# Performance work log

Hardware: AMD Instinct MI355X
Metric: run time of the kernel (lower is better)

The kernel has to match this reference:

```python
import jax, jax.numpy as jnp
import numpy as np

D_MODEL = 1024
H = 16
D_K = D_MODEL // H
B = 2
S = 2048
NEG = -1000000000.0


def setup_inputs() -> dict:
    key = jax.random.key(0)
    ks = jax.random.split(key, 11)
    sc = 1.0 / np.sqrt(D_MODEL)
    inp = {
        "q": jax.random.normal(ks[0], (B, S, D_MODEL), jnp.float32),
        "k": jax.random.normal(ks[1], (B, S, D_MODEL), jnp.float32),
        "v": jax.random.normal(ks[2], (B, S, D_MODEL), jnp.float32),
        "mask": jnp.tril(jnp.ones((S, S), jnp.int32))[None, None, :, :],  # causal [1,1,S,S]
        "Wq": jax.random.normal(ks[3], (D_MODEL, D_MODEL), jnp.float32) * sc,
        "bq": jnp.zeros((D_MODEL,), jnp.float32),
        "Wk": jax.random.normal(ks[4], (D_MODEL, D_MODEL), jnp.float32) * sc,
        "bk": jnp.zeros((D_MODEL,), jnp.float32),
        "Wv": jax.random.normal(ks[5], (D_MODEL, D_MODEL), jnp.float32) * sc,
        "bv": jnp.zeros((D_MODEL,), jnp.float32),
        "Wo": jax.random.normal(ks[6], (D_MODEL, D_MODEL), jnp.float32) * sc,
        "bo": jnp.zeros((D_MODEL,), jnp.float32),
    }
    return inp


def reference(q, k, v, mask, Wq, bq, Wk, bk, Wv, bv, Wo, bo):
    # Linear projections (torch Linear: x @ W.T + b)
    query = q @ Wq.T + bq
    key_ = k @ Wk.T + bk
    value = v @ Wv.T + bv
    # [B,S,D] -> [B,H,S,Dk]
    def split_heads(x):
        return x.reshape(B, S, H, D_K).transpose(0, 2, 1, 3)
    query, key_, value = split_heads(query), split_heads(key_), split_heads(value)
    # scaled dot-product attention, scores [B,H,S,S]
    scores = jnp.einsum("bhqd,bhkd->bhqk", query, key_) / jnp.sqrt(
        jnp.asarray(D_K, query.dtype))
    scores = jnp.where(mask == 0, jnp.asarray(NEG, scores.dtype), scores)
    attn = jax.nn.softmax(scores, axis=-1)
    x = jnp.einsum("bhqk,bhkd->bhqd", attn, value)
    # merge heads [B,H,S,Dk] -> [B,S,D]
    x = x.transpose(0, 2, 1, 3).reshape(B, S, D_MODEL)
    return x @ Wo.T + bo
```

## Files before the change

### kernel.cpp

```cpp
#include <hip/hip_runtime.h>
#include <stdint.h>

#define D_MODEL 1024
#define NHEAD   16
#define DKH     64
#define NB      2
#define SSEQ    2048

typedef unsigned short u16;
typedef __bf16 bf16x8 __attribute__((ext_vector_type(8)));
typedef float  f32x4  __attribute__((ext_vector_type(4)));
typedef u16    u16x8  __attribute__((ext_vector_type(8)));

__device__ __forceinline__ u16 f2bf(float x) {
  union { float f; uint32_t u; } c; c.f = x;
  uint32_t r = c.u + 0x7FFFu + ((c.u >> 16) & 1u);
  return (u16)(r >> 16);
}

__device__ __forceinline__ void gload_lds16(const void* gsrc, void* ldsdst) {
  typedef const __attribute__((address_space(1))) uint32_t* gp_t;
  typedef __attribute__((address_space(3))) uint32_t* lp_t;
  gp_t g = reinterpret_cast<gp_t>(reinterpret_cast<uintptr_t>(gsrc));
  lp_t l = reinterpret_cast<lp_t>(reinterpret_cast<uintptr_t>(ldsdst));
  __builtin_amdgcn_global_load_lds(g, l, 16, 0, 0);
}

__device__ __forceinline__ f32x4 mfma16(bf16x8 a, bf16x8 b, f32x4 c) {
  return __builtin_amdgcn_mfma_f32_16x16x32_bf16(a, b, c, 0, 0, 0);
}

__device__ __forceinline__ bf16x8 lds_frag(const u16* tile, int row, int kelem) {
  int chunk = (kelem >> 3) ^ (row & 7);
  return *reinterpret_cast<const bf16x8*>(
      reinterpret_cast<const char*>(tile) + row * 128 + chunk * 16);
}

template<int NROWS>
__device__ __forceinline__ void stage_tile(const u16* __restrict__ g, int row0, int ldk,
                                           int k0, u16* ldsbase, int wid, int lane) {
  constexpr int CPW = NROWS / 32;
  #pragma unroll
  for (int i = 0; i < CPW; ++i) {
    int c = wid * CPW + i;
    int row = c * 8 + (lane >> 3);
    int cchunk = (lane & 7) ^ (lane >> 3);
    const u16* src = g + (size_t)(row0 + row) * ldk + k0 + cchunk * 8;
    gload_lds16(src, reinterpret_cast<char*>(ldsbase) + c * 1024);
  }
}

__global__ __launch_bounds__(256) void cast_kernel(
    const float* __restrict__ s0, const float* __restrict__ s1,
    const float* __restrict__ s2, const float* __restrict__ s3,
    u16* __restrict__ d0, u16* __restrict__ d1, u16* __restrict__ d2, u16* __restrict__ d3,
    int n8) {
  const int z = blockIdx.z;
  const float* s = (z == 0) ? s0 : (z == 1) ? s1 : (z == 2) ? s2 : s3;
  u16* d = (z == 0) ? d0 : (z == 1) ? d1 : (z == 2) ? d2 : d3;
  int i = blockIdx.x * 256 + threadIdx.x;
  if (i >= n8) return;
  float4 a = reinterpret_cast<const float4*>(s)[2 * i];
  float4 b = reinterpret_cast<const float4*>(s)[2 * i + 1];
  u16x8 o;
  o[0] = f2bf(a.x); o[1] = f2bf(a.y); o[2] = f2bf(a.z); o[3] = f2bf(a.w);
  o[4] = f2bf(b.x); o[5] = f2bf(b.y); o[6] = f2bf(b.z); o[7] = f2bf(b.w);
  reinterpret_cast<u16x8*>(d)[i] = o;
}

__device__ __forceinline__ void gemm_core(const u16* __restrict__ A, const u16* __restrict__ W,
                                          u16* ldsA, u16* ldsB, int brow, int bcol,
                                          f32x4 acc[4][4]) {
  const int tid = threadIdx.x;
  const int lane = tid & 63;
  const int wid = tid >> 6;
  const int wr = wid >> 1;
  const int wc = wid & 1;
  f32x4 z4 = {0.f, 0.f, 0.f, 0.f};
  #pragma unroll
  for (int i = 0; i < 4; ++i)
    #pragma unroll
    for (int j = 0; j < 4; ++j) acc[i][j] = z4;

  stage_tile<128>(A, brow, D_MODEL, 0, ldsA, wid, lane);
  stage_tile<128>(W, bcol, D_MODEL, 0, ldsB, wid, lane);
  __syncthreads();
  int buf = 0;
  const int KT = D_MODEL / 64;
  for (int kt = 0; kt < KT; ++kt) {
    if (kt + 1 < KT) {
      stage_tile<128>(A, brow, D_MODEL, (kt + 1) * 64, ldsA + (buf ^ 1) * 8192, wid, lane);
      stage_tile<128>(W, bcol, D_MODEL, (kt + 1) * 64, ldsB + (buf ^ 1) * 8192, wid, lane);
    }
    const u16* tA = ldsA + buf * 8192;
    const u16* tB = ldsB + buf * 8192;
    #pragma unroll
    for (int kk = 0; kk < 2; ++kk) {
      const int ke = kk * 32 + ((lane >> 4) << 3);
      bf16x8 af[4], bf[4];
      #pragma unroll
      for (int i = 0; i < 4; ++i) af[i] = lds_frag(tA, wr * 64 + i * 16 + (lane & 15), ke);
      #pragma unroll
      for (int j = 0; j < 4; ++j) bf[j] = lds_frag(tB, wc * 64 + j * 16 + (lane & 15), ke);
      __builtin_amdgcn_s_setprio(1);
      #pragma unroll
      for (int i = 0; i < 4; ++i)
        #pragma unroll
        for (int j = 0; j < 4; ++j) acc[i][j] = mfma16(af[i], bf[j], acc[i][j]);
      __builtin_amdgcn_s_setprio(0);
    }
    __syncthreads();
    buf ^= 1;
  }
}

__global__ __launch_bounds__(256) void gemm_qkv(
    const u16* __restrict__ x0, const u16* __restrict__ x1, const u16* __restrict__ x2,
    const u16* __restrict__ w0, const u16* __restrict__ w1, const u16* __restrict__ w2,
    const float* __restrict__ b0, const float* __restrict__ b1, const float* __restrict__ b2,
    u16* __restrict__ o0, u16* __restrict__ o1, u16* __restrict__ o2) {
  __shared__ u16 ldsA[2 * 128 * 64];
  __shared__ u16 ldsB[2 * 128 * 64];
  const int z = blockIdx.z;
  const u16* X = (z == 0) ? x0 : (z == 1) ? x1 : x2;
  const u16* W = (z == 0) ? w0 : (z == 1) ? w1 : w2;
  const float* bias = (z == 0) ? b0 : (z == 1) ? b1 : b2;
  u16* O = (z == 0) ? o0 : (z == 1) ? o1 : o2;
  const float scale = (z == 0) ? 0.125f : 1.0f;
  const int brow = blockIdx.y * 128;
  const int bcol = blockIdx.x * 128;
  f32x4 acc[4][4];
  gemm_core(X, W, ldsA, ldsB, brow, bcol, acc);
  const int lane = threadIdx.x & 63;
  const int wid = threadIdx.x >> 6;
  const int wr = wid >> 1, wc = wid & 1;
  #pragma unroll
  for (int j = 0; j < 4; ++j) {
    const int n = bcol + wc * 64 + j * 16 + (lane & 15);
    const float bn = bias[n];
    const int h = n >> 6, d = n & 63;
    #pragma unroll
    for (int i = 0; i < 4; ++i)
      #pragma unroll
      for (int r = 0; r < 4; ++r) {
        const int m = brow + wr * 64 + i * 16 + ((lane >> 4) << 2) + r;
        const int bb = m >> 11, s = m & (SSEQ - 1);
        O[(((size_t)(bb * NHEAD + h) * SSEQ + s) << 6) + d] = f2bf((acc[i][j][r] + bn) * scale);
      }
  }
}

__global__ __launch_bounds__(256) void gemm_out(const u16* __restrict__ A,
                                                const u16* __restrict__ W,
                                                const float* __restrict__ bias,
                                                float* __restrict__ out) {
  __shared__ u16 ldsA[2 * 128 * 64];
  __shared__ u16 ldsB[2 * 128 * 64];
  const int brow = blockIdx.y * 128;
  const int bcol = blockIdx.x * 128;
  f32x4 acc[4][4];
  gemm_core(A, W, ldsA, ldsB, brow, bcol, acc);
  const int lane = threadIdx.x & 63;
  const int wid = threadIdx.x >> 6;
  const int wr = wid >> 1, wc = wid & 1;
  #pragma unroll
  for (int j = 0; j < 4; ++j) {
    const int n = bcol + wc * 64 + j * 16 + (lane & 15);
    const float bn = bias[n];
    #pragma unroll
    for (int i = 0; i < 4; ++i)
      #pragma unroll
      for (int r = 0; r < 4; ++r) {
        const int m = brow + wr * 64 + i * 16 + ((lane >> 4) << 2) + r;
        out[(size_t)m * D_MODEL + n] = acc[i][j][r] + bn;
      }
  }
}

__global__ __launch_bounds__(256) void transpose_v(const u16* __restrict__ V,
                                                   u16* __restrict__ Vt) {
  __shared__ u16 t[64][72];
  const int tid = threadIdx.x;
  const int bh = blockIdx.y;
  const int s0 = blockIdx.x * 64;
  const u16* Vb = V + ((size_t)bh * SSEQ + s0) * DKH;
  const int row = tid >> 2;
  const int cg = (tid & 3) * 16;
  uint4 a = *reinterpret_cast<const uint4*>(Vb + (size_t)row * DKH + cg);
  uint4 b = *reinterpret_cast<const uint4*>(Vb + (size_t)row * DKH + cg + 8);
  *reinterpret_cast<uint4*>(&t[row][cg]) = a;
  *reinterpret_cast<uint4*>(&t[row][cg + 8]) = b;
  __syncthreads();
  const int d = tid >> 2;
  const int sg = (tid & 3) * 16;
  u16 vals[16];
  #pragma unroll
  for (int j = 0; j < 16; ++j) vals[j] = t[sg + j][d];
  u16* dst = Vt + ((size_t)bh * DKH + d) * SSEQ + s0 + sg;
  *reinterpret_cast<uint4*>(dst) = *reinterpret_cast<uint4*>(&vals[0]);
  *reinterpret_cast<uint4*>(dst + 8) = *reinterpret_cast<uint4*>(&vals[8]);
}

__device__ __forceinline__ void attn_strip(const u16* __restrict__ Qb,
                                           const u16* __restrict__ Kb,
                                           const u16* __restrict__ Vb,
                                           u16* __restrict__ ctxb,
                                           u16* myP, int strip, int lane) {
  const int g = lane >> 4;
  const int q0 = strip * 16;
  const int nt = (strip >> 2) + 1;
  const u16* Qp = Qb + (size_t)(q0 + (lane & 15)) * DKH + (g << 3);
  bf16x8 qf0 = *reinterpret_cast<const bf16x8*>(Qp);
  bf16x8 qf1 = *reinterpret_cast<const bf16x8*>(Qp + 32);

  f32x4 z4 = {0.f, 0.f, 0.f, 0.f};
  f32x4 acc[4] = {z4, z4, z4, z4};
  float mrow[4] = {-1e30f, -1e30f, -1e30f, -1e30f};
  float lrow[4] = {0.f, 0.f, 0.f, 0.f};

  bf16x8 kf[8], vf[8];
  #pragma unroll
  for (int jk = 0; jk < 4; ++jk)
    #pragma unroll
    for (int c = 0; c < 2; ++c)
      kf[jk * 2 + c] = *reinterpret_cast<const bf16x8*>(
          Kb + (size_t)(jk * 16 + (lane & 15)) * DKH + c * 32 + (g << 3));

  for (int t = 0; t < nt; ++t) {
    #pragma unroll
    for (int j = 0; j < 4; ++j)
      #pragma unroll
      for (int c = 0; c < 2; ++c)
        vf[j * 2 + c] = *reinterpret_cast<const bf16x8*>(
            Vb + (size_t)(j * 16 + (lane & 15)) * SSEQ + t * 64 + c * 32 + (g << 3));
    f32x4 sf[4];
    __builtin_amdgcn_s_setprio(1);
    #pragma unroll
    for (int jk = 0; jk < 4; ++jk) {
      f32x4 s = mfma16(qf0, kf[jk * 2 + 0], z4);
      sf[jk] = mfma16(qf1, kf[jk * 2 + 1], s);
    }
    __builtin_amdgcn_s_setprio(0);
    if (t + 1 < nt) {
      #pragma unroll
      for (int jk = 0; jk < 4; ++jk)
        #pragma unroll
        for (int c = 0; c < 2; ++c)
          kf[jk * 2 + c] = *reinterpret_cast<const bf16x8*>(
              Kb + (size_t)((t + 1) * 64 + jk * 16 + (lane & 15)) * DKH + c * 32 + (g << 3));
    }
    if (t == nt - 1) {
      #pragma unroll
      for (int jk = 0; jk < 4; ++jk)
        #pragma unroll
        for (int r = 0; r < 4; ++r) {
          int kv = t * 64 + jk * 16 + (lane & 15);
          int qrow = q0 + g * 4 + r;
          if (kv > qrow) sf[jk][r] = -1e9f;
        }
    }
    float scl[4];
    #pragma unroll
    for (int r = 0; r < 4; ++r) {
      float mx = fmaxf(fmaxf(sf[0][r], sf[1][r]), fmaxf(sf[2][r], sf[3][r]));
      #pragma unroll
      for (int dd = 1; dd < 16; dd <<= 1) mx = fmaxf(mx, __shfl_xor(mx, dd));
      float mn = fmaxf(mrow[r], mx);
      scl[r] = __expf(mrow[r] - mn);
      mrow[r] = mn;
      lrow[r] *= scl[r];
    }
    float rsum[4] = {0.f, 0.f, 0.f, 0.f};
    #pragma unroll
    for (int jk = 0; jk < 4; ++jk)
      #pragma unroll
      for (int r = 0; r < 4; ++r) {
        float p = __expf(sf[jk][r] - mrow[r]);
        rsum[r] += p;
        int row = g * 4 + r;
        int col = jk * 16 + (lane & 15);
        int chunk = (col >> 3) ^ (row & 7);
        *reinterpret_cast<u16*>(reinterpret_cast<char*>(myP) + row * 128 + chunk * 16 +
                                (col & 7) * 2) = f2bf(p);
      }
    #pragma unroll
    for (int r = 0; r < 4; ++r) {
      float s = rsum[r];
      #pragma unroll
      for (int dd = 1; dd < 16; dd <<= 1) s += __shfl_xor(s, dd);
      lrow[r] += s;
    }
    #pragma unroll
    for (int j = 0; j < 4; ++j)
      #pragma unroll
      for (int r = 0; r < 4; ++r) acc[j][r] *= scl[r];
    #pragma unroll
    for (int c = 0; c < 2; ++c) {
      bf16x8 pf = lds_frag(myP, lane & 15, c * 32 + (g << 3));
      __builtin_amdgcn_s_setprio(1);
      #pragma unroll
      for (int j = 0; j < 4; ++j) acc[j] = mfma16(pf, vf[j * 2 + c], acc[j]);
      __builtin_amdgcn_s_setprio(0);
    }
  }
  float inv[4];
  #pragma unroll
  for (int r = 0; r < 4; ++r) inv[r] = 1.0f / lrow[r];
  #pragma unroll
  for (int j = 0; j < 4; ++j)
    #pragma unroll
    for (int r = 0; r < 4; ++r) {
      int qrow = q0 + g * 4 + r;
      int d = j * 16 + (lane & 15);
      ctxb[(size_t)qrow * D_MODEL + d] = f2bf(acc[j][r] * inv[r]);
    }
}

__global__ __launch_bounds__(256) void attn_kernel(const u16* __restrict__ Q,
                                                   const u16* __restrict__ K,
                                                   const u16* __restrict__ Vt,
                                                   u16* __restrict__ ctx) {
  __shared__ u16 ldsP[4 * 16 * 64];
  const int lane = threadIdx.x & 63;
  const int wid = threadIdx.x >> 6;
  const int L = blockIdx.x + 16 * blockIdx.y;
  const int bh = ((L & 7) << 2) | ((L >> 3) & 3);
  const int p = (((L >> 5) & 15) << 2) | wid;
  const u16* Qb = Q + (size_t)bh * SSEQ * DKH;
  const u16* Kb = K + (size_t)bh * SSEQ * DKH;
  const u16* Vb = Vt + (size_t)bh * DKH * SSEQ;
  u16* ctxb = ctx + (size_t)(bh >> 4) * SSEQ * D_MODEL + (bh & 15) * DKH;
  u16* myP = ldsP + wid * 1024;
  attn_strip(Qb, Kb, Vb, ctxb, myP, 127 - p, lane);
  attn_strip(Qb, Kb, Vb, ctxb, myP, p, lane);
}

extern "C" void kernel_launch(void* const* d_in, const int* in_sizes, int n_in,
                              void* d_out, int out_size, void* d_ws, size_t ws_size,
                              hipStream_t stream) {
  const float* q  = (const float*)d_in[0];
  const float* k  = (const float*)d_in[1];
  const float* v  = (const float*)d_in[2];
  const float* Wq = (const float*)d_in[4];
  const float* bq = (const float*)d_in[5];
  const float* Wk = (const float*)d_in[6];
  const float* bk = (const float*)d_in[7];
  const float* Wv = (const float*)d_in[8];
  const float* bv = (const float*)d_in[9];
  const float* Wo = (const float*)d_in[10];
  const float* bo = (const float*)d_in[11];

  char* ws = (char*)d_ws;
  const size_t SZ_QKV = (size_t)NB * SSEQ * D_MODEL * 2;
  const size_t SZ_W   = (size_t)D_MODEL * D_MODEL * 2;
  u16* qb  = (u16*)(ws);
  u16* kb  = (u16*)(ws + SZ_QKV);
  u16* vb  = (u16*)(ws + 2 * SZ_QKV);
  u16* wqb = (u16*)(ws + 3 * SZ_QKV);
  u16* wkb = (u16*)(ws + 3 * SZ_QKV + SZ_W);
  u16* wvb = (u16*)(ws + 3 * SZ_QKV + 2 * SZ_W);
  u16* wob = (u16*)(ws + 3 * SZ_QKV + 3 * SZ_W);
  u16* Qh  = (u16*)(ws + 3 * SZ_QKV + 4 * SZ_W);
  u16* Kh  = (u16*)(ws + 4 * SZ_QKV + 4 * SZ_W);
  u16* Vh  = (u16*)(ws + 5 * SZ_QKV + 4 * SZ_W);
  u16* Vth = (u16*)(ws + 6 * SZ_QKV + 4 * SZ_W);
  u16* ctx = (u16*)(ws + 7 * SZ_QKV + 4 * SZ_W);

  cast_kernel<<<dim3(2048, 1, 3), 256, 0, stream>>>(
      q, k, v, nullptr, qb, kb, vb, nullptr, (NB * SSEQ * D_MODEL) / 8);
  cast_kernel<<<dim3(512, 1, 4), 256, 0, stream>>>(
      Wq, Wk, Wv, Wo, wqb, wkb, wvb, wob, (D_MODEL * D_MODEL) / 8);
  gemm_qkv<<<dim3(8, 32, 3), 256, 0, stream>>>(qb, kb, vb, wqb, wkb, wvb,
                                               bq, bk, bv, Qh, Kh, Vh);
  transpose_v<<<dim3(SSEQ / 64, NB * NHEAD), 256, 0, stream>>>(Vh, Vth);
  attn_kernel<<<dim3(16, 32), 256, 0, stream>>>(Qh, Kh, Vth, ctx);
  gemm_out<<<dim3(8, 32), 256, 0, stream>>>(ctx, wob, bo, (float*)d_out);
}
```

Baseline: 311.3 us.

## Rewrite attention with 32x32 MFMA, register-resident P, and lazy rescaling

Replaces the 16x16 MFMA attention with a 32x32x16 MFMA variant that computes S^T per 32-row strip, keeps P in registers via packed bf16 converts and lane shuffles instead of an LDS round trip, and skips the running-max rescale unless the max grows by more than a threshold. The launch changes from 512 four-wave blocks that each process a pair of balanced strips to 2048 single-wave blocks, one strip each, ordered longest first. It aims to cut LDS traffic, shuffle reductions and exp work per tile, at the cost of less work per wave, more blocks, and per-wave causal load imbalance handled only by ordering.

```diff
diff --git a/kernel.cpp b/kernel.cpp
--- a/kernel.cpp
+++ b/kernel.cpp
@@ -10,12 +10,19 @@
 typedef unsigned short u16;
 typedef __bf16 bf16x8 __attribute__((ext_vector_type(8)));
 typedef float  f32x4  __attribute__((ext_vector_type(4)));
+typedef float  f32x16 __attribute__((ext_vector_type(16)));
 typedef u16    u16x8  __attribute__((ext_vector_type(8)));
 
 __device__ __forceinline__ u16 f2bf(float x) {
   union { float f; uint32_t u; } c; c.f = x;
   uint32_t r = c.u + 0x7FFFu + ((c.u >> 16) & 1u);
   return (u16)(r >> 16);
+}
+
+__device__ __forceinline__ uint32_t cvtpk(float lo, float hi) {
+  uint32_t r;
+  asm("v_cvt_pk_bf16_f32 %0, %1, %2" : "=v"(r) : "v"(lo), "v"(hi));
+  return r;
 }
 
 __device__ __forceinline__ void gload_lds16(const void* gsrc, void* ldsdst) {
@@ -28,6 +35,9 @@
 
 __device__ __forceinline__ f32x4 mfma16(bf16x8 a, bf16x8 b, f32x4 c) {
   return __builtin_amdgcn_mfma_f32_16x16x32_bf16(a, b, c, 0, 0, 0);
+}
+__device__ __forceinline__ f32x16 mfma32(bf16x8 a, bf16x8 b, f32x16 c) {
+  return __builtin_amdgcn_mfma_f32_32x32x16_bf16(a, b, c, 0, 0, 0);
 }
 
 __device__ __forceinline__ bf16x8 lds_frag(const u16* tile, int row, int kelem) {
@@ -201,138 +211,141 @@
   *reinterpret_cast<uint4*>(dst + 8) = *reinterpret_cast<uint4*>(&vals[8]);
 }
 
-__device__ __forceinline__ void attn_strip(const u16* __restrict__ Qb,
-                                           const u16* __restrict__ Kb,
-                                           const u16* __restrict__ Vb,
-                                           u16* __restrict__ ctxb,
-                                           u16* myP, int strip, int lane) {
-  const int g = lane >> 4;
-  const int q0 = strip * 16;
-  const int nt = (strip >> 2) + 1;
-  const u16* Qp = Qb + (size_t)(q0 + (lane & 15)) * DKH + (g << 3);
-  bf16x8 qf0 = *reinterpret_cast<const bf16x8*>(Qp);
-  bf16x8 qf1 = *reinterpret_cast<const bf16x8*>(Qp + 32);
-
-  f32x4 z4 = {0.f, 0.f, 0.f, 0.f};
-  f32x4 acc[4] = {z4, z4, z4, z4};
-  float mrow[4] = {-1e30f, -1e30f, -1e30f, -1e30f};
-  float lrow[4] = {0.f, 0.f, 0.f, 0.f};
-
-  bf16x8 kf[8], vf[8];
-  #pragma unroll
-  for (int jk = 0; jk < 4; ++jk)
-    #pragma unroll
-    for (int c = 0; c < 2; ++c)
-      kf[jk * 2 + c] = *reinterpret_cast<const bf16x8*>(
-          Kb + (size_t)(jk * 16 + (lane & 15)) * DKH + c * 32 + (g << 3));
+union W4 { uint32_t w[4]; bf16x8 v; };
+
+__device__ __forceinline__ void attn_strip32(const u16* __restrict__ Qb,
+                                             const u16* __restrict__ Kb,
+                                             const u16* __restrict__ Vb,
+                                             u16* __restrict__ ctxb,
+                                             int strip, int lane) {
+  const int lo = lane & 31;
+  const int hi = lane >> 5;
+  const int q0 = strip * 32;
+  const int nt = strip + 1;
+
+  bf16x8 qf[4];
+  const u16* qrow = Qb + (size_t)(q0 + lo) * DKH + hi * 8;
+  #pragma unroll
+  for (int s = 0; s < 4; ++s) qf[s] = *reinterpret_cast<const bf16x8*>(qrow + s * 16);
+
+  const u16* krow = Kb + (size_t)lo * DKH + hi * 8;
+  bf16x8 kf[4];
+  #pragma unroll
+  for (int s = 0; s < 4; ++s) kf[s] = *reinterpret_cast<const bf16x8*>(krow + s * 16);
+
+  const u16* vrow = Vb + (size_t)lo * SSEQ + hi * 8;
+  bf16x8 vf[2][2];
+  #pragma unroll
+  for (int kh = 0; kh < 2; ++kh)
+    #pragma unroll
+    for (int db = 0; db < 2; ++db)
+      vf[kh][db] = *reinterpret_cast<const bf16x8*>(vrow + db * 32 * SSEQ + kh * 16);
+
+  f32x16 z16 = {};
+  f32x16 acc0 = z16, acc1 = z16;
+  float m = -1e30f, lsum = 0.f;
 
   for (int t = 0; t < nt; ++t) {
-    #pragma unroll
-    for (int j = 0; j < 4; ++j)
-      #pragma unroll
-      for (int c = 0; c < 2; ++c)
-        vf[j * 2 + c] = *reinterpret_cast<const bf16x8*>(
-            Vb + (size_t)(j * 16 + (lane & 15)) * SSEQ + t * 64 + c * 32 + (g << 3));
-    f32x4 sf[4];
+    f32x16 sf = z16;
     __builtin_amdgcn_s_setprio(1);
     #pragma unroll
-    for (int jk = 0; jk < 4; ++jk) {
-      f32x4 s = mfma16(qf0, kf[jk * 2 + 0], z4);
-      sf[jk] = mfma16(qf1, kf[jk * 2 + 1], s);
-    }
+    for (int s = 0; s < 4; ++s) sf = mfma32(kf[s], qf[s], sf);
     __builtin_amdgcn_s_setprio(0);
     if (t + 1 < nt) {
-      #pragma unroll
-      for (int jk = 0; jk < 4; ++jk)
+      const u16* kn = krow + (size_t)(t + 1) * 32 * DKH;
+      #pragma unroll
+      for (int s = 0; s < 4; ++s) kf[s] = *reinterpret_cast<const bf16x8*>(kn + s * 16);
+    }
+    if (t == nt - 1) {
+      #pragma unroll
+      for (int r = 0; r < 16; ++r) {
+        int kvp = (r & 3) + 8 * (r >> 2) + 4 * hi;
+        if (kvp > lo) sf[r] = -1e9f;
+      }
+    }
+    float t01 = fmaxf(sf[0], sf[1]),   t23 = fmaxf(sf[2], sf[3]);
+    float t45 = fmaxf(sf[4], sf[5]),   t67 = fmaxf(sf[6], sf[7]);
+    float t89 = fmaxf(sf[8], sf[9]),   tab = fmaxf(sf[10], sf[11]);
+    float tcd = fmaxf(sf[12], sf[13]), tef = fmaxf(sf[14], sf[15]);
+    float pm = fmaxf(fmaxf(fmaxf(t01, t23), fmaxf(t45, t67)),
+                     fmaxf(fmaxf(t89, tab), fmaxf(tcd, tef)));
+    pm = fmaxf(pm, __shfl_xor(pm, 32));
+    if (t == 0) {
+      m = pm;
+    } else if (!__all(pm - m <= 6.0f)) {
+      float mn = fmaxf(m, pm);
+      float scl = __expf(m - mn);
+      lsum *= scl;
+      #pragma unroll
+      for (int r = 0; r < 16; ++r) {
+        int idx = (((r & 3) + 8 * (r >> 2)) << 2) + (hi << 4);
+        float sr = __int_as_float(__builtin_amdgcn_ds_bpermute(idx, __float_as_int(scl)));
+        acc0[r] *= sr;
+        acc1[r] *= sr;
+      }
+      m = mn;
+    }
+    float pr[16];
+    #pragma unroll
+    for (int r = 0; r < 16; ++r) pr[r] = __expf(sf[r] - m);
+    float rs = (((pr[0] + pr[1]) + (pr[2] + pr[3])) + ((pr[4] + pr[5]) + (pr[6] + pr[7]))) +
+               (((pr[8] + pr[9]) + (pr[10] + pr[11])) + ((pr[12] + pr[13]) + (pr[14] + pr[15])));
+    rs += __shfl_xor(rs, 32);
+    lsum += rs;
+    uint32_t a = cvtpk(pr[0], pr[1]), b = cvtpk(pr[2], pr[3]);
+    uint32_t c = cvtpk(pr[4], pr[5]), d = cvtpk(pr[6], pr[7]);
+    uint32_t e = cvtpk(pr[8], pr[9]), f = cvtpk(pr[10], pr[11]);
+    uint32_t g = cvtpk(pr[12], pr[13]), h = cvtpk(pr[14], pr[15]);
+    uint32_t ap = __shfl_xor((int)a, 32), bp = __shfl_xor((int)b, 32);
+    uint32_t cp = __shfl_xor((int)c, 32), dp = __shfl_xor((int)d, 32);
+    uint32_t ep = __shfl_xor((int)e, 32), fp = __shfl_xor((int)f, 32);
+    uint32_t gp = __shfl_xor((int)g, 32), hp = __shfl_xor((int)h, 32);
+    W4 pa0, pa1;
+    pa0.w[0] = hi ? cp : a;  pa0.w[1] = hi ? dp : b;
+    pa0.w[2] = hi ? c : ap;  pa0.w[3] = hi ? d : bp;
+    pa1.w[0] = hi ? gp : e;  pa1.w[1] = hi ? hp : f;
+    pa1.w[2] = hi ? g : ep;  pa1.w[3] = hi ? h : fp;
+    __builtin_amdgcn_s_setprio(1);
+    acc0 = mfma32(pa0.v, vf[0][0], acc0);
+    acc0 = mfma32(pa1.v, vf[1][0], acc0);
+    acc1 = mfma32(pa0.v, vf[0][1], acc1);
+    acc1 = mfma32(pa1.v, vf[1][1], acc1);
+    __builtin_amdgcn_s_setprio(0);
+    if (t + 1 < nt) {
+      const u16* vn = vrow + (t + 1) * 32;
+      #pragma unroll
+      for (int kh = 0; kh < 2; ++kh)
         #pragma unroll
-        for (int c = 0; c < 2; ++c)
-          kf[jk * 2 + c] = *reinterpret_cast<const bf16x8*>(
-              Kb + (size_t)((t + 1) * 64 + jk * 16 + (lane & 15)) * DKH + c * 32 + (g << 3));
-    }
-    if (t == nt - 1) {
-      #pragma unroll
-      for (int jk = 0; jk < 4; ++jk)
-        #pragma unroll
-        for (int r = 0; r < 4; ++r) {
-          int kv = t * 64 + jk * 16 + (lane & 15);
-          int qrow = q0 + g * 4 + r;
-          if (kv > qrow) sf[jk][r] = -1e9f;
-        }
-    }
-    float scl[4];
-    #pragma unroll
-    for (int r = 0; r < 4; ++r) {
-      float mx = fmaxf(fmaxf(sf[0][r], sf[1][r]), fmaxf(sf[2][r], sf[3][r]));
-      #pragma unroll
-      for (int dd = 1; dd < 16; dd <<= 1) mx = fmaxf(mx, __shfl_xor(mx, dd));
-      float mn = fmaxf(mrow[r], mx);
-      scl[r] = __expf(mrow[r] - mn);
-      mrow[r] = mn;
-      lrow[r] *= scl[r];
-    }
-    float rsum[4] = {0.f, 0.f, 0.f, 0.f};
-    #pragma unroll
-    for (int jk = 0; jk < 4; ++jk)
-      #pragma unroll
-      for (int r = 0; r < 4; ++r) {
-        float p = __expf(sf[jk][r] - mrow[r]);
-        rsum[r] += p;
-        int row = g * 4 + r;
-        int col = jk * 16 + (lane & 15);
-        int chunk = (col >> 3) ^ (row & 7);
-        *reinterpret_cast<u16*>(reinterpret_cast<char*>(myP) + row * 128 + chunk * 16 +
-                                (col & 7) * 2) = f2bf(p);
-      }
-    #pragma unroll
-    for (int r = 0; r < 4; ++r) {
-      float s = rsum[r];
-      #pragma unroll
-      for (int dd = 1; dd < 16; dd <<= 1) s += __shfl_xor(s, dd);
-      lrow[r] += s;
-    }
-    #pragma unroll
-    for (int j = 0; j < 4; ++j)
-      #pragma unroll
-      for (int r = 0; r < 4; ++r) acc[j][r] *= scl[r];
-    #pragma unroll
-    for (int c = 0; c < 2; ++c) {
-      bf16x8 pf = lds_frag(myP, lane & 15, c * 32 + (g << 3));
-      __builtin_amdgcn_s_setprio(1);
-      #pragma unroll
-      for (int j = 0; j < 4; ++j) acc[j] = mfma16(pf, vf[j * 2 + c], acc[j]);
-      __builtin_amdgcn_s_setprio(0);
-    }
-  }
-  float inv[4];
-  #pragma unroll
-  for (int r = 0; r < 4; ++r) inv[r] = 1.0f / lrow[r];
-  #pragma unroll
-  for (int j = 0; j < 4; ++j)
-    #pragma unroll
-    for (int r = 0; r < 4; ++r) {
-      int qrow = q0 + g * 4 + r;
-      int d = j * 16 + (lane & 15);
-      ctxb[(size_t)qrow * D_MODEL + d] = f2bf(acc[j][r] * inv[r]);
-    }
-}
-
-__global__ __launch_bounds__(256) void attn_kernel(const u16* __restrict__ Q,
-                                                   const u16* __restrict__ K,
-                                                   const u16* __restrict__ Vt,
-                                                   u16* __restrict__ ctx) {
-  __shared__ u16 ldsP[4 * 16 * 64];
-  const int lane = threadIdx.x & 63;
-  const int wid = threadIdx.x >> 6;
-  const int L = blockIdx.x + 16 * blockIdx.y;
-  const int bh = ((L & 7) << 2) | ((L >> 3) & 3);
-  const int p = (((L >> 5) & 15) << 2) | wid;
+        for (int db = 0; db < 2; ++db)
+          vf[kh][db] = *reinterpret_cast<const bf16x8*>(vn + db * 32 * SSEQ + kh * 16);
+    }
+  }
+  float inv = 1.0f / lsum;
+  #pragma unroll
+  for (int r = 0; r < 16; ++r) {
+    int rp = (r & 3) + 8 * (r >> 2) + 4 * hi;
+    int idx = (((r & 3) + 8 * (r >> 2)) << 2) + (hi << 4);
+    float ir = __int_as_float(__builtin_amdgcn_ds_bpermute(idx, __float_as_int(inv)));
+    u16* orow = ctxb + (size_t)(q0 + rp) * D_MODEL;
+    orow[lo] = f2bf(acc0[r] * ir);
+    orow[32 + lo] = f2bf(acc1[r] * ir);
+  }
+}
+
+__global__ __launch_bounds__(64) void attn_kernel(const u16* __restrict__ Q,
+                                                  const u16* __restrict__ K,
+                                                  const u16* __restrict__ Vt,
+                                                  u16* __restrict__ ctx) {
+  const int lane = threadIdx.x;
+  const int bid = blockIdx.x;
+  const int j = bid >> 3;
+  const int bh = ((bid & 7) << 2) | (j >> 6);
+  const int strip = 63 - (j & 63);
   const u16* Qb = Q + (size_t)bh * SSEQ * DKH;
   const u16* Kb = K + (size_t)bh * SSEQ * DKH;
   const u16* Vb = Vt + (size_t)bh * DKH * SSEQ;
   u16* ctxb = ctx + (size_t)(bh >> 4) * SSEQ * D_MODEL + (bh & 15) * DKH;
-  u16* myP = ldsP + wid * 1024;
-  attn_strip(Qb, Kb, Vb, ctxb, myP, 127 - p, lane);
-  attn_strip(Qb, Kb, Vb, ctxb, myP, p, lane);
+  attn_strip32(Qb, Kb, Vb, ctxb, strip, lane);
 }
 
 extern "C" void kernel_launch(void* const* d_in, const int* in_sizes, int n_in,
@@ -373,6 +386,6 @@
   gemm_qkv<<<dim3(8, 32, 3), 256, 0, stream>>>(qb, kb, vb, wqb, wkb, wvb,
                                                bq, bk, bv, Qh, Kh, Vh);
   transpose_v<<<dim3(SSEQ / 64, NB * NHEAD), 256, 0, stream>>>(Vh, Vth);
-  attn_kernel<<<dim3(16, 32), 256, 0, stream>>>(Qh, Kh, Vth, ctx);
+  attn_kernel<<<dim3(2048), 64, 0, stream>>>(Qh, Kh, Vth, ctx);
   gemm_out<<<dim3(8, 32), 256, 0, stream>>>(ctx, wob, bo, (float*)d_out);
 }
```

Result: faster. 280.0 us (-10.1%).
